# Optimization experiments

Measured on AMD Instinct MI355X. Metric: run time of the kernel, lower is better.

## Reference

```python
import jax, jax.numpy as jnp
import numpy as np


def _forward(data_vecs, data_weights, data_biases, edge_weights, edge_biases,
             score_weights, data, types, graphs, edges, pos):
    data = np.asarray(data); types = np.asarray(types)
    graphs = np.asarray(graphs); edges = np.asarray(edges).copy()
    pos = int(pos)
    edges[pos] = -1  # forward() mutation: score the pos edge over ALL edge types
    n = int(data.shape[0]); G = int(graphs.shape[0]); dim = data_weights.shape[-1]

    # base (leaf) embeddings for all nodes at once: [n, dim]
    sel = data_vecs[types, data]  # [n, vec_dim] embedding-table gather
    base = jnp.einsum('nv,nvd->nd', sel, data_weights[types]) + data_biases[types]

    def add_child(emb, ce, e):
        # emb/ce: [dim] or [E, dim]; e < 0 -> broadcast child over all edge types
        if e < 0:
            contrib = jnp.einsum('d,edf->ef', ce, edge_weights) + edge_biases
        else:
            contrib = ce @ edge_weights[e] + edge_biases[e]
        return emb + contrib  # broadcasting [dim] + [E,dim] mirrors torch's cat-expand

    scores = []
    for g in range(G):
        parents = graphs[g].copy()
        roots = [i for i in range(n) if parents[i] == i]
        for i in range(len(roots) - 1):  # chain multiple roots (no-op for single root)
            parents[roots[i]] = roots[i + 1]
        root = roots[-1]
        parents[root] = -n
        children = {}
        for c in range(n):
            p = int(parents[c])
            if p >= 0:
                children.setdefault(p, []).append(c)
        denom = float(len(children) + 1)  # faithful to source: len of whole dict

        def rec(idx):
            emb = base[idx]
            if idx not in children:
                return emb
            for c in children[idx]:
                emb = add_child(emb, rec(c), int(edges[c]))
            return jnp.maximum(emb / denom, 0.0)

        emb = rec(root)
        final = add_child(jnp.zeros((dim,), base.dtype), emb, int(edges[root]))
        scores.append((final @ score_weights)[:, 0])  # [E]
    return jnp.stack(scores)  # [G, E]


def setup_inputs():
    T, V, VD, DIM, E = 2, 100000, 512, 512, 64
    N, G = 128, 16
    ks = jax.random.split(jax.random.key(0), 6)
    s = DIM ** -0.5  # keep recursion numerically stable (torch.rand init would overflow)
    inp = {
        'data_vecs': jax.random.normal(ks[0], (T, V, VD), jnp.float32),
        'data_weights': jax.random.uniform(ks[1], (T, VD, DIM), jnp.float32) * s,
        'data_biases': jax.random.uniform(ks[2], (T, DIM), jnp.float32) * s,
        'edge_weights': jax.random.uniform(ks[3], (E, DIM, DIM), jnp.float32) * s,
        'edge_biases': jax.random.uniform(ks[4], (E, DIM), jnp.float32) * s,
        'score_weights': jax.random.uniform(ks[5], (DIM, 1), jnp.float32) * s,
    }
    rng = np.random.RandomState(0)
    inp['data'] = rng.randint(0, V, size=N).astype(np.int64)
    inp['types'] = rng.randint(0, T, size=N).astype(np.int64)
    graphs = np.zeros((G, N), dtype=np.int64)
    for g in range(G):
        for i in range(1, N):
            graphs[g, i] = rng.randint(0, i)  # random tree; node 0 self-parent = root
    inp['graphs'] = graphs
    inp['edges'] = rng.randint(0, E, size=N).astype(np.int64)
    inp['pos'] = 5
    return inp


def reference(data_vecs, data_weights, data_biases, edge_weights, edge_biases,
              score_weights, data, types, graphs, edges, pos):
    return _forward(data_vecs, data_weights, data_biases, edge_weights,
                    edge_biases, score_weights, data, types, graphs, edges, pos)
```

## Files before the change

### kernel.cpp

```cpp
#include <hip/hip_runtime.h>

#define DIMC 512
#define NMAX 128

__global__ __launch_bounds__(256)
void base_kernel(const float* __restrict__ data_vecs,
                 const float* __restrict__ data_weights,
                 const float* __restrict__ data_biases,
                 const int* __restrict__ data,
                 const int* __restrict__ types,
                 float* __restrict__ base,
                 int V, int VD) {
  const int n = blockIdx.x;
  const int t = threadIdx.x;
  __shared__ float sel[DIMC];
  const int ty = types[n];
  const long long idx = data[n];
  const float* src = data_vecs + ((long long)ty * V + idx) * VD;
  for (int d = t; d < VD; d += 256) sel[d] = src[d];
  __syncthreads();
  const float* W = data_weights + (long long)ty * VD * DIMC;
  const int f0 = 2 * t;
  float2 a = {0.f, 0.f};
  #pragma unroll 16
  for (int d = 0; d < VD; ++d) {
    const float s = sel[d];
    const float2 w = *(const float2*)(W + (long long)d * DIMC + f0);
    a.x = fmaf(s, w.x, a.x);
    a.y = fmaf(s, w.y, a.y);
  }
  const float* b = data_biases + (long long)ty * DIMC;
  base[(long long)n * DIMC + f0]     = a.x + b[f0];
  base[(long long)n * DIMC + f0 + 1] = a.y + b[f0 + 1];
}

__global__ __launch_bounds__(NMAX)
void setup_kernel(const int* __restrict__ graphs,
                  const int* __restrict__ edges,
                  const int* __restrict__ pos_p,
                  int* __restrict__ par, int* __restrict__ onp,
                  int* __restrict__ chOff, int* __restrict__ chList,
                  int* __restrict__ plist,
                  int* __restrict__ plen, int* __restrict__ eroot,
                  float* __restrict__ inv_denom,
                  int G, int N) {
  const int g = blockIdx.x;
  const int t = threadIdx.x;
  __shared__ int P[NMAX], C[NMAX], O[NMAX], CO[NMAX + 1];
  __shared__ int s_root;
  if (t < N) { P[t] = graphs[g * N + t]; C[t] = 0; O[t] = 0; }
  __syncthreads();
  if (t == 0) {
    int prev = -1;
    for (int i = 0; i < N; ++i)
      if (P[i] == i) { if (prev >= 0) P[prev] = i; prev = i; }
    s_root = prev;
    P[prev] = -1;
  }
  __syncthreads();
  const int root = s_root;
  if (t < N) { const int p = P[t]; if (p >= 0) atomicAdd(&C[p], 1); }
  __syncthreads();
  if (t == 0) {
    int internal = 0, acc = 0;
    for (int c = 0; c < N; ++c) {
      CO[c] = acc; acc += C[c];
      if (C[c] > 0) internal++;
    }
    CO[N] = acc;
    inv_denom[g] = 1.0f / (float)(internal + 1);
  }
  __syncthreads();
  if (t < N) {
    const int p = P[t];
    if (p >= 0) {
      int r = 0;
      for (int c = 0; c < t; ++c) if (P[c] == p) ++r;
      chList[g * N + CO[p] + r] = t;
    }
  }
  if (t == 0) {
    const int pos = *pos_p;
    int pl = 0;
    int x = (pos == root) ? -1 : P[pos];
    while (x >= 0) { plist[g * N + pl++] = x; O[x] = 1; x = P[x]; }
    plen[g] = pl;
    eroot[g] = (root == pos) ? -1 : edges[root];
  }
  __syncthreads();
  if (t < N) {
    par[g * N + t] = P[t];
    onp[g * N + t] = O[t];
    chOff[g * (N + 1) + t] = CO[t];
  }
  if (t == 0) chOff[g * (N + 1) + N] = CO[N];
}

__global__ __launch_bounds__(512)
void score_prep_kernel(const float* __restrict__ ew, const float* __restrict__ eb,
                       const float* __restrict__ sw_g,
                       const int* __restrict__ eroot,
                       float* __restrict__ u, float* __restrict__ c0) {
  const int g = blockIdx.x >> 3;
  const int chunk = blockIdx.x & 7;
  const int t = threadIdx.x;
  const int wave = t >> 6;
  const int lane = t & 63;
  __shared__ float sw[DIMC];
  sw[t] = sw_g[t];
  __syncthreads();
  const int er = eroot[g];
  if (er < 0) { if (t == 0 && chunk == 0) c0[g] = 0.f; return; }
  const float* Wb = ew + (long long)er * DIMC * DIMC;
  #pragma unroll
  for (int rr = 0; rr < 8; ++rr) {
    const int r = chunk * 64 + wave * 8 + rr;
    const float* row = Wb + (long long)r * DIMC;
    float a = 0.f;
    #pragma unroll
    for (int k = 0; k < 8; ++k)
      a = fmaf(row[lane + 64 * k], sw[lane + 64 * k], a);
    #pragma unroll
    for (int off = 32; off > 0; off >>= 1) a += __shfl_down(a, off, 64);
    if (lane == 0) u[(long long)g * DIMC + r] = a;
  }
  if (chunk == 0) {
    __shared__ float red[512];
    red[t] = eb[(long long)er * DIMC + t] * sw[t];
    __syncthreads();
    for (int s = 256; s > 0; s >>= 1) {
      if (t < s) red[t] += red[t + s];
      __syncthreads();
    }
    if (t == 0) c0[g] = red[0];
  }
}

__device__ __forceinline__ float agent_ld(const float* p) {
  return __hip_atomic_load((float*)p, __ATOMIC_RELAXED, __HIP_MEMORY_SCOPE_AGENT);
}
__device__ __forceinline__ void agent_st(float* p, float v) {
  __hip_atomic_store(p, v, __ATOMIC_RELAXED, __HIP_MEMORY_SCOPE_AGENT);
}

struct P1Args {
  const float* base; float* epos; float* contrib;
  const float* ew; const float* eb;
  const int* par; const int* onp;
  const int* chOff; const int* chList;
  const int* edges; const float* invd; const int* pos_p;
  int* ready;
  int G, N;
};

__global__ __launch_bounds__(128, 4)
void pass1_flags(P1Args p) {
  const int b = blockIdx.x;
  const int g = b / p.N;
  const int c = p.N - 1 - (b - g * p.N);
  const int gi = g * p.N + c;
  if (p.onp[gi]) return;
  const int t = threadIdx.x;
  const int f0 = 4 * t;
  __shared__ float v[DIMC];
  __shared__ int go;
  const int pos = *p.pos_p;
  const int pr = p.par[gi];
  const float inv = p.invd[g];
  const int cs   = p.chOff[g * (p.N + 1) + c];
  const int cend = p.chOff[g * (p.N + 1) + c + 1];
  const bool will_mm = (c != pos && pr >= 0);
  const int e = p.edges[c];
  const float* W = p.ew + (long long)e * DIMC * DIMC;

  if (cend > cs) {
    if (t == 0) go = 0;
    __syncthreads();
    if (t == 0) {
      for (int k = cs; k < cend; ++k) {
        const int ch = p.chList[g * p.N + k];
        while (__hip_atomic_load(p.ready + (g * p.N + ch), __ATOMIC_RELAXED,
                                 __HIP_MEMORY_SCOPE_AGENT) == 0)
          __builtin_amdgcn_s_sleep(2);
      }
      __hip_atomic_store(&go, 1, __ATOMIC_RELAXED,
                         __HIP_MEMORY_SCOPE_WORKGROUP);
    } else if (t >= 64 && will_mm) {
      float dummy = 0.f;
      const int ti = t - 64;
      for (int chunk = 0; chunk < 32; ++chunk) {
        #pragma unroll
        for (int k = 0; k < 8; ++k) {
          const int line = chunk * 512 + k * 64 + ti;
          dummy += W[(long long)line * 16];
        }
        if (__hip_atomic_load(&go, __ATOMIC_RELAXED,
                              __HIP_MEMORY_SCOPE_WORKGROUP)) break;
      }
      asm volatile("" :: "v"(dummy));
    }
    __syncthreads();
  }

  const float* bs = p.base + (long long)c * DIMC;
  float4 val = *(const float4*)(bs + f0);
  if (cend > cs) {
    for (int k = cs; k < cend; ++k) {
      const int ch = p.chList[g * p.N + k];
      const float* cv = p.contrib + ((long long)g * p.N + ch) * DIMC;
      val.x += agent_ld(cv + f0);
      val.y += agent_ld(cv + f0 + 1);
      val.z += agent_ld(cv + f0 + 2);
      val.w += agent_ld(cv + f0 + 3);
    }
    val.x = fmaxf(val.x * inv, 0.f);
    val.y = fmaxf(val.y * inv, 0.f);
    val.z = fmaxf(val.z * inv, 0.f);
    val.w = fmaxf(val.w * inv, 0.f);
  }
  if (c == pos)
    *(float4*)(p.epos + (long long)g * DIMC + f0) = val;
  v[f0] = val.x; v[f0 + 1] = val.y; v[f0 + 2] = val.z; v[f0 + 3] = val.w;
  __syncthreads();

  if (will_mm) {
    float4 a = {0.f, 0.f, 0.f, 0.f};
    #pragma unroll 16
    for (int d = 0; d < DIMC; ++d) {
      const float s = v[d];
      const float4 w = *(const float4*)(W + (long long)d * DIMC + f0);
      a.x = fmaf(s, w.x, a.x);
      a.y = fmaf(s, w.y, a.y);
      a.z = fmaf(s, w.z, a.z);
      a.w = fmaf(s, w.w, a.w);
    }
    const float4 bb = *(const float4*)(p.eb + (long long)e * DIMC + f0);
    float* cv = p.contrib + ((long long)g * p.N + c) * DIMC;
    agent_st(cv + f0,     a.x + bb.x);
    agent_st(cv + f0 + 1, a.y + bb.y);
    agent_st(cv + f0 + 2, a.z + bb.z);
    agent_st(cv + f0 + 3, a.w + bb.w);
  }
  __syncthreads();
  if (t == 0) {
    asm volatile("s_waitcnt vmcnt(0)" ::: "memory");
    __hip_atomic_store(p.ready + gi, 1, __ATOMIC_RELAXED,
                       __HIP_MEMORY_SCOPE_AGENT);
  }
}

struct P2Args {
  const float* base; const float* epos; const float* contrib;
  const float* ew; const float* eb; const float* sw;
  const float* u; const float* c0; const float* inv_denom;
  const int* plist; const int* plen; const int* edges; const int* pos_p;
  const int* chOff; const int* chList; const int* onp;
  float* out; int G, N, E;
};

__global__ __launch_bounds__(512)
void pass2_kernel(P2Args p) {
  const int g = blockIdx.x / p.E;
  const int e = blockIdx.x - g * p.E;
  const int t = threadIdx.x;
  const int dg = t >> 7;
  const int tl = t & 127;
  const int f0 = 4 * tl;
  __shared__ float ce[DIMC];
  __shared__ float part[4][DIMC];
  __shared__ float red[512];
  const int pos = *p.pos_p;
  ce[t] = p.epos[(long long)g * DIMC + t];
  __syncthreads();
  const int pl = p.plen[g];
  const float inv = p.inv_denom[g];
  for (int s = 0; s < pl; ++s) {
    const int pnode = p.plist[g * p.N + s];
    const int we = (s == 0) ? e : p.edges[p.plist[g * p.N + s - 1]];
    const float* W = p.ew + (long long)we * DIMC * DIMC
                   + (long long)(dg * 128) * DIMC;
    float4 a = {0.f, 0.f, 0.f, 0.f};
    #pragma unroll 16
    for (int i = 0; i < 128; ++i) {
      const float sv = ce[dg * 128 + i];
      const float4 w = *(const float4*)(W + (long long)i * DIMC + f0);
      a.x = fmaf(sv, w.x, a.x);
      a.y = fmaf(sv, w.y, a.y);
      a.z = fmaf(sv, w.z, a.z);
      a.w = fmaf(sv, w.w, a.w);
    }
    part[dg][f0]     = a.x;
    part[dg][f0 + 1] = a.y;
    part[dg][f0 + 2] = a.z;
    part[dg][f0 + 3] = a.w;
    __syncthreads();
    float sum = part[0][t] + part[1][t] + part[2][t] + part[3][t]
              + p.eb[(long long)we * DIMC + t]
              + p.base[(long long)pnode * DIMC + t];
    const int cs   = p.chOff[g * (p.N + 1) + pnode];
    const int cend = p.chOff[g * (p.N + 1) + pnode + 1];
    for (int k = cs; k < cend; ++k) {
      const int ch = p.chList[g * p.N + k];
      if (ch == pos || p.onp[g * p.N + ch]) continue;
      sum += p.contrib[((long long)g * p.N + ch) * DIMC + t];
    }
    sum = fmaxf(sum * inv, 0.f);
    __syncthreads();
    ce[t] = sum;
    __syncthreads();
  }
  float partial;
  if (pl > 0) {
    partial = ce[t] * p.u[(long long)g * DIMC + t];
  } else {
    const float* W = p.ew + (long long)e * DIMC * DIMC
                   + (long long)(dg * 128) * DIMC;
    float4 a = {0.f, 0.f, 0.f, 0.f};
    #pragma unroll 16
    for (int i = 0; i < 128; ++i) {
      const float sv = ce[dg * 128 + i];
      const float4 w = *(const float4*)(W + (long long)i * DIMC + f0);
      a.x = fmaf(sv, w.x, a.x);
      a.y = fmaf(sv, w.y, a.y);
      a.z = fmaf(sv, w.z, a.z);
      a.w = fmaf(sv, w.w, a.w);
    }
    part[dg][f0]     = a.x;
    part[dg][f0 + 1] = a.y;
    part[dg][f0 + 2] = a.z;
    part[dg][f0 + 3] = a.w;
    __syncthreads();
    const float fin = part[0][t] + part[1][t] + part[2][t] + part[3][t]
                    + p.eb[(long long)e * DIMC + t];
    partial = fin * p.sw[t];
  }
  red[t] = partial;
  __syncthreads();
  for (int s2 = 256; s2 > 0; s2 >>= 1) {
    if (t < s2) red[t] += red[t + s2];
    __syncthreads();
  }
  if (t == 0) {
    p.out[(long long)g * p.E + e] = red[0] + ((pl > 0) ? p.c0[g] : 0.f);
  }
}

extern "C" void kernel_launch(void* const* d_in, const int* in_sizes, int n_in,
                              void* d_out, int out_size, void* d_ws, size_t ws_size,
                              hipStream_t stream) {
  const float* data_vecs    = (const float*)d_in[0];
  const float* data_weights = (const float*)d_in[1];
  const float* data_biases  = (const float*)d_in[2];
  const float* edge_weights = (const float*)d_in[3];
  const float* edge_biases  = (const float*)d_in[4];
  const float* score_w      = (const float*)d_in[5];
  const int*   data   = (const int*)d_in[6];
  const int*   types  = (const int*)d_in[7];
  const int*   graphs = (const int*)d_in[8];
  const int*   edges  = (const int*)d_in[9];
  const int*   pos_p  = (const int*)d_in[10];

  const int DIM = in_sizes[5];
  const int T   = in_sizes[2] / DIM;
  const int E   = in_sizes[4] / DIM;
  const int N   = in_sizes[6];
  const int G   = in_sizes[8] / N;
  const int VD  = in_sizes[1] / (T * DIM);
  const int V   = in_sizes[0] / (T * VD);
  (void)DIM; (void)n_in; (void)ws_size; (void)out_size;

  char* w = (char*)d_ws;
  float* base    = (float*)w;   w += (size_t)N * DIMC * sizeof(float);
  float* epos    = (float*)w;   w += (size_t)G * DIMC * sizeof(float);
  float* contrib = (float*)w;   w += (size_t)G * N * DIMC * sizeof(float);
  float* u       = (float*)w;   w += (size_t)G * DIMC * sizeof(float);
  float* c0      = (float*)w;   w += (size_t)G * sizeof(float);
  float* invd    = (float*)w;   w += (size_t)G * sizeof(float);
  int* par    = (int*)w;        w += (size_t)G * N * sizeof(int);
  int* onp    = (int*)w;        w += (size_t)G * N * sizeof(int);
  int* chOff  = (int*)w;        w += (size_t)G * (N + 1) * sizeof(int);
  int* chList = (int*)w;        w += (size_t)G * N * sizeof(int);
  int* plist  = (int*)w;        w += (size_t)G * N * sizeof(int);
  int* plen   = (int*)w;        w += (size_t)G * sizeof(int);
  int* eroot  = (int*)w;        w += (size_t)G * sizeof(int);
  int* ready  = (int*)w;        w += (size_t)G * N * sizeof(int);

  hipMemsetAsync(ready, 0, (size_t)G * N * sizeof(int), stream);

  base_kernel<<<N, 256, 0, stream>>>(data_vecs, data_weights, data_biases,
                                     data, types, base, V, VD);

  setup_kernel<<<G, NMAX, 0, stream>>>(graphs, edges, pos_p,
                                       par, onp, chOff, chList,
                                       plist, plen, eroot, invd, G, N);

  score_prep_kernel<<<G * 8, 512, 0, stream>>>(edge_weights, edge_biases,
                                               score_w, eroot, u, c0);

  P1Args p1;
  p1.base = base; p1.epos = epos; p1.contrib = contrib;
  p1.ew = edge_weights; p1.eb = edge_biases;
  p1.par = par; p1.onp = onp;
  p1.chOff = chOff; p1.chList = chList;
  p1.edges = edges; p1.invd = invd; p1.pos_p = pos_p;
  p1.ready = ready;
  p1.G = G; p1.N = N;
  pass1_flags<<<G * N, 128, 0, stream>>>(p1);

  P2Args p2;
  p2.base = base; p2.epos = epos; p2.contrib = contrib;
  p2.ew = edge_weights; p2.eb = edge_biases; p2.sw = score_w;
  p2.u = u; p2.c0 = c0; p2.inv_denom = invd;
  p2.plist = plist; p2.plen = plen; p2.edges = edges; p2.pos_p = pos_p;
  p2.chOff = chOff; p2.chList = chList; p2.onp = onp;
  p2.out = (float*)d_out; p2.G = G; p2.N = N; p2.E = E;
  pass2_kernel<<<G * E, 512, 0, stream>>>(p2);
}
```

Baseline: 980.3 us.

## Split pass1 matvec reduction dimension across two thread halves and drop prefetch

Pass1 blocks grow from 128 to 256 threads. Each half computes a partial matvec over half of the 512-long reduction dimension, and the two partials are summed through shared memory before the contrib store. The speculative W-prefetch loop that ran while waiting on child readiness flags is removed. This halves the serial dependent chain length per tree node on the critical path, at the cost of an extra sync and no warm-up of the 1 MB weight matrix during the wait.

```diff
diff --git a/kernel.cpp b/kernel.cpp
--- a/kernel.cpp
+++ b/kernel.cpp
@@ -153,7 +153,7 @@
   int G, N;
 };
 
-__global__ __launch_bounds__(128, 4)
+__global__ __launch_bounds__(256, 8)
 void pass1_flags(P1Args p) {
   const int b = blockIdx.x;
   const int g = b / p.N;
@@ -161,9 +161,12 @@
   const int gi = g * p.N + c;
   if (p.onp[gi]) return;
   const int t = threadIdx.x;
-  const int f0 = 4 * t;
+  const int dg = t >> 7;
+  const int tl = t & 127;
+  const int f0 = 4 * tl;
+  const int f2 = 2 * t;
   __shared__ float v[DIMC];
-  __shared__ int go;
+  __shared__ float part[2][DIMC];
   const int pos = *p.pos_p;
   const int pr = p.par[gi];
   const float inv = p.invd[g];
@@ -174,8 +177,6 @@
   const float* W = p.ew + (long long)e * DIMC * DIMC;
 
   if (cend > cs) {
-    if (t == 0) go = 0;
-    __syncthreads();
     if (t == 0) {
       for (int k = cs; k < cend; ++k) {
         const int ch = p.chList[g * p.N + k];
@@ -183,63 +184,55 @@
                                  __HIP_MEMORY_SCOPE_AGENT) == 0)
           __builtin_amdgcn_s_sleep(2);
       }
-      __hip_atomic_store(&go, 1, __ATOMIC_RELAXED,
-                         __HIP_MEMORY_SCOPE_WORKGROUP);
-    } else if (t >= 64 && will_mm) {
-      float dummy = 0.f;
-      const int ti = t - 64;
-      for (int chunk = 0; chunk < 32; ++chunk) {
-        #pragma unroll
-        for (int k = 0; k < 8; ++k) {
-          const int line = chunk * 512 + k * 64 + ti;
-          dummy += W[(long long)line * 16];
-        }
-        if (__hip_atomic_load(&go, __ATOMIC_RELAXED,
-                              __HIP_MEMORY_SCOPE_WORKGROUP)) break;
+    }
+    __syncthreads();
+  }
+
+  {
+    const float* bs = p.base + (long long)c * DIMC;
+    float vx = bs[f2], vy = bs[f2 + 1];
+    if (cend > cs) {
+      for (int k = cs; k < cend; ++k) {
+        const int ch = p.chList[g * p.N + k];
+        const float* cv = p.contrib + ((long long)g * p.N + ch) * DIMC;
+        vx += agent_ld(cv + f2);
+        vy += agent_ld(cv + f2 + 1);
       }
-      asm volatile("" :: "v"(dummy));
-    }
-    __syncthreads();
-  }
-
-  const float* bs = p.base + (long long)c * DIMC;
-  float4 val = *(const float4*)(bs + f0);
-  if (cend > cs) {
-    for (int k = cs; k < cend; ++k) {
-      const int ch = p.chList[g * p.N + k];
-      const float* cv = p.contrib + ((long long)g * p.N + ch) * DIMC;
-      val.x += agent_ld(cv + f0);
-      val.y += agent_ld(cv + f0 + 1);
-      val.z += agent_ld(cv + f0 + 2);
-      val.w += agent_ld(cv + f0 + 3);
-    }
-    val.x = fmaxf(val.x * inv, 0.f);
-    val.y = fmaxf(val.y * inv, 0.f);
-    val.z = fmaxf(val.z * inv, 0.f);
-    val.w = fmaxf(val.w * inv, 0.f);
-  }
-  if (c == pos)
-    *(float4*)(p.epos + (long long)g * DIMC + f0) = val;
-  v[f0] = val.x; v[f0 + 1] = val.y; v[f0 + 2] = val.z; v[f0 + 3] = val.w;
+      vx = fmaxf(vx * inv, 0.f);
+      vy = fmaxf(vy * inv, 0.f);
+    }
+    if (c == pos) {
+      p.epos[(long long)g * DIMC + f2]     = vx;
+      p.epos[(long long)g * DIMC + f2 + 1] = vy;
+    }
+    v[f2] = vx; v[f2 + 1] = vy;
+  }
   __syncthreads();
 
   if (will_mm) {
+    const float* Wg = W + (long long)(dg * 256) * DIMC;
     float4 a = {0.f, 0.f, 0.f, 0.f};
     #pragma unroll 16
-    for (int d = 0; d < DIMC; ++d) {
-      const float s = v[d];
-      const float4 w = *(const float4*)(W + (long long)d * DIMC + f0);
+    for (int i = 0; i < 256; ++i) {
+      const float s = v[dg * 256 + i];
+      const float4 w = *(const float4*)(Wg + (long long)i * DIMC + f0);
       a.x = fmaf(s, w.x, a.x);
       a.y = fmaf(s, w.y, a.y);
       a.z = fmaf(s, w.z, a.z);
       a.w = fmaf(s, w.w, a.w);
     }
-    const float4 bb = *(const float4*)(p.eb + (long long)e * DIMC + f0);
+    part[dg][f0]     = a.x;
+    part[dg][f0 + 1] = a.y;
+    part[dg][f0 + 2] = a.z;
+    part[dg][f0 + 3] = a.w;
+    __syncthreads();
+    const float sx = part[0][f2]     + part[1][f2]
+                   + p.eb[(long long)e * DIMC + f2];
+    const float sy = part[0][f2 + 1] + part[1][f2 + 1]
+                   + p.eb[(long long)e * DIMC + f2 + 1];
     float* cv = p.contrib + ((long long)g * p.N + c) * DIMC;
-    agent_st(cv + f0,     a.x + bb.x);
-    agent_st(cv + f0 + 1, a.y + bb.y);
-    agent_st(cv + f0 + 2, a.z + bb.z);
-    agent_st(cv + f0 + 3, a.w + bb.w);
+    agent_st(cv + f2,     sx);
+    agent_st(cv + f2 + 1, sy);
   }
   __syncthreads();
   if (t == 0) {
@@ -405,7 +398,7 @@
   p1.edges = edges; p1.invd = invd; p1.pos_p = pos_p;
   p1.ready = ready;
   p1.G = G; p1.N = N;
-  pass1_flags<<<G * N, 128, 0, stream>>>(p1);
+  pass1_flags<<<G * N, 256, 0, stream>>>(p1);
 
   P2Args p2;
   p2.base = base; p2.epos = epos; p2.contrib = contrib;
```

New measurement: 1.272 ms. 1.3x slower.
